# Optimization experiments

Hardware: AMD Instinct MI355X
Metric: run time of the kernel (lower is better)

Reference implementation:

```python
import jax, jax.numpy as jnp
import numpy as np

N, D, H, DZ, R, K, M = 50000, 256, 4, 64, 4, 32, 2
NE, NT = 1600000, 100000
LAM2, LAM3, LAMM = 1.0, 0.5, 1.0
BETA2, BETA3, BETAM = 1.0, 1.0, 1.0
GCLIP, SCLIP, DAMP, EPS = 1.0, 10.0, 0.9999, 1e-5


def _ln(x, gamma, bias):
    mu = x.mean(-1, keepdims=True)
    v = ((x - mu) ** 2).mean(-1, keepdims=True)
    return gamma * (x - mu) / jnp.sqrt(v + EPS) + bias


def _seg_lse(s, idx, n):
    # segment logsumexp over rows of s [E,H] grouped by idx -> [n,H]; 0 for empty segments
    m = jnp.full((n,) + s.shape[1:], -jnp.inf, s.dtype).at[idx].max(s)
    ms = jnp.where(jnp.isfinite(m), m, 0.0)
    z = jnp.zeros((n,) + s.shape[1:], s.dtype).at[idx].add(jnp.exp(s - ms[idx]))
    return jnp.where(z > 0, ms + jnp.log(jnp.maximum(z, 1e-30)), 0.0)


def _energy(X, gamma, bias, W_Q2, W_K2, W_Q3, W_K3, T_tau, W_Qm, W_Km, B_mem,
            c2, u2, c3, u3, v3, tt):
    G = _ln(X, gamma, bias)
    # pairwise (2nd order) attention energy over edges
    Q2 = jnp.einsum('nd,hzd->nhz', G, W_Q2)
    K2 = jnp.einsum('nd,hzd->nhz', G, W_K2)
    s2 = BETA2 * jnp.einsum('ehz,ehz->eh', Q2[c2], K2[u2])
    e = -(LAM2 / BETA2) * _seg_lse(s2, c2, N).sum()
    # motif (3rd order) energy over triples with learned motif tensor T_tau
    Q3 = jnp.einsum('nd,hzd->nhz', G, W_Q3).reshape(N, H, R, DZ)
    K3 = jnp.einsum('nd,hzd->nhz', G, W_K3).reshape(N, H, R, DZ)
    s3 = BETA3 * jnp.einsum('thrz,thrz,thrz,thrz->th', Q3[c3], K3[u3], K3[v3], T_tau[tt])
    e += -(LAM3 / BETA3) * _seg_lse(s3, c3, N).sum()
    # Hopfield-style memory retrieval energy
    Qm = jnp.einsum('nd,hzd->nhz', G, W_Qm)
    Km = jnp.einsum('kd,hzd->hkz', B_mem, W_Km)
    sm = BETAM * jnp.einsum('nhz,hkz->nhk', Qm, Km)
    e += -(LAMM / BETAM) * jax.nn.logsumexp(sm, axis=-1).sum()
    return e


def setup_inputs():
    key = jax.random.key(0)
    ks = jax.random.split(key, 16)
    xav2 = (2.0 / (DZ + D)) ** 0.5
    xav3 = 0.5 * (2.0 / (R * DZ + D)) ** 0.5
    return {
        'X': jax.random.normal(ks[0], (N, D), jnp.float32),
        'c2': jax.random.randint(ks[1], (NE,), 0, N),
        'u2': jax.random.randint(ks[2], (NE,), 0, N),
        'c3': jax.random.randint(ks[3], (NT,), 0, N),
        'u3': jax.random.randint(ks[4], (NT,), 0, N),
        'v3': jax.random.randint(ks[5], (NT,), 0, N),
        't_tau': jax.random.randint(ks[6], (NT,), 0, M),
        'batch': jnp.zeros((N,), jnp.int64) if jax.config.jax_enable_x64 else jnp.zeros((N,), jnp.int32),
        'step_size': jnp.ones((), jnp.float32),
        'gamma': jnp.ones((D,), jnp.float32),
        'bias': jnp.zeros((D,), jnp.float32),
        'W_Q2': jax.random.normal(ks[7], (H, DZ, D), jnp.float32) * xav2,
        'W_K2': jax.random.normal(ks[8], (H, DZ, D), jnp.float32) * xav2,
        'W_Q3': jax.random.normal(ks[9], (H, R * DZ, D), jnp.float32) * xav3,
        'W_K3': jax.random.normal(ks[10], (H, R * DZ, D), jnp.float32) * xav3,
        'T_tau': jax.random.normal(ks[11], (M, H, R, DZ), jnp.float32) * 0.02,
        'W_Qm': jax.random.normal(ks[12], (H, DZ, D), jnp.float32) * 0.5 * xav2,
        'W_Km': jax.random.normal(ks[13], (H, DZ, D), jnp.float32) * 0.5 * xav2,
        'B_mem': jax.random.normal(ks[14], (K, D), jnp.float32) / (D ** 0.5),
    }


def reference(X, c2, u2, c3, u3, v3, t_tau, batch, step_size, gamma, bias,
              W_Q2, W_K2, W_Q3, W_K3, T_tau, W_Qm, W_Km, B_mem):
    E, gX = jax.value_and_grad(_energy)(
        X, gamma, bias, W_Q2, W_K2, W_Q3, W_K3, T_tau, W_Qm, W_Km, B_mem,
        c2, u2, c3, u3, v3, t_tau)
    gn = jnp.linalg.norm(gX, axis=-1, keepdims=True)
    gX = gX * (GCLIP / jnp.maximum(gn, GCLIP))
    Xn = X - step_size * DAMP * gX
    sn = jnp.linalg.norm(Xn, axis=-1, keepdims=True)
    Xn = Xn * (SCLIP / jnp.maximum(sn, SCLIP))
    return Xn, E
```

## Files before the change

### kernel.cpp

```cpp
#include <hip/hip_runtime.h>
#include <math.h>

#define N_NODES 50000
#define D_DIM   256
#define H_HEADS 4
#define NE_EDGES 1600000
#define NT_TRIS  100000

#define LAM2  1.0f
#define LAM3  0.5f
#define LAMM  1.0f
#define GCLIP 1.0f
#define SCLIP 10.0f
#define DAMP  0.9999f
#define EPSLN 1e-5f

typedef short bf16x8 __attribute__((ext_vector_type(8)));
typedef float f32x4  __attribute__((ext_vector_type(4)));

__device__ __forceinline__ float b2f(unsigned short u) {
  return __uint_as_float(((unsigned)u) << 16);
}
__device__ __forceinline__ unsigned short f2b(float f) {
  unsigned u = __float_as_uint(f);
  return (unsigned short)((u + 0x7fffu + ((u >> 16) & 1u)) >> 16);
}
__device__ __forceinline__ bf16x8 ld8(const unsigned short* p) {
  union { uint4 u; bf16x8 v; } t;
  t.u = *(const uint4*)p;
  return t.v;
}
__device__ __forceinline__ void ld4f(const unsigned short* p, float* o) {
  uint2 t = *(const uint2*)p;
  o[0] = __uint_as_float((t.x & 0xffffu) << 16);
  o[1] = __uint_as_float((t.x >> 16) << 16);
  o[2] = __uint_as_float((t.y & 0xffffu) << 16);
  o[3] = __uint_as_float((t.y >> 16) << 16);
}

__device__ __forceinline__ float bsum256(float v, volatile float* red) {
  #pragma unroll
  for (int o = 32; o; o >>= 1) v += __shfl_xor(v, o);
  __syncthreads();
  if ((threadIdx.x & 63) == 0) red[threadIdx.x >> 6] = v;
  __syncthreads();
  return red[0] + red[1] + red[2] + red[3];
}

__global__ void zero_buf(float* __restrict__ p, long n) {
  long i = ((long)blockIdx.x * blockDim.x + threadIdx.x) * 4;
  if (i + 3 < n) *(float4*)(p + i) = make_float4(0.f, 0.f, 0.f, 0.f);
  else for (long j = i; j < n; j++) p[j] = 0.f;
}

__global__ __launch_bounds__(256) void ln_fwd(const float* __restrict__ X,
    float* __restrict__ mu_out, float* __restrict__ rstd_out) {
  __shared__ float red[4];
  int n = blockIdx.x, t = threadIdx.x;
  float x = X[(size_t)n * D_DIM + t];
  float mu = bsum256(x, red) * (1.0f / D_DIM);
  float d = x - mu;
  float var = bsum256(d * d, red) * (1.0f / D_DIM);
  if (t == 0) { mu_out[n] = mu; rstd_out[n] = rsqrtf(var + EPSLN); }
}

__global__ void km_build(const float* __restrict__ Bmem, const float* __restrict__ WKm,
                         float* __restrict__ Km) {
  int idx = blockIdx.x * blockDim.x + threadIdx.x;
  if (idx >= 4 * 32 * 64) return;
  int h = idx >> 11, k = (idx >> 6) & 31, z = idx & 63;
  const float* b = Bmem + (size_t)k * D_DIM;
  const float* w = WKm + ((size_t)h * 64 + z) * D_DIM;
  float s = 0.f;
  for (int d = 0; d < D_DIM; d++) s += b[d] * w[d];
  Km[idx] = s;
}

__global__ void conv_all(const float* __restrict__ WQ2, const float* __restrict__ WK2,
                         const float* __restrict__ WQ3, const float* __restrict__ WK3,
                         const float* __restrict__ WQm,
                         unsigned short* __restrict__ wb, unsigned short* __restrict__ wbt) {
  int i = blockIdx.x * 256 + threadIdx.x;
  int r = i >> 8, d = i & 255;
  const float* src; int lr;
  if (r < 256)       { src = WQ2; lr = r; }
  else if (r < 512)  { src = WK2; lr = r - 256; }
  else if (r < 1536) { src = WQ3; lr = r - 512; }
  else if (r < 2560) { src = WK3; lr = r - 1536; }
  else               { src = WQm; lr = r - 2560; }
  unsigned short v = f2b(src[(size_t)lr * 256 + d]);
  wb[i] = v;
  wbt[(((size_t)(r >> 6) * 256 + d) << 6) + (r & 63)] = v;
}

__global__ void hist5(const int* __restrict__ c2, const int* __restrict__ u2,
                      const int* __restrict__ c3, const int* __restrict__ u3,
                      const int* __restrict__ v3, int* __restrict__ cnt) {
  long i = (long)blockIdx.x * blockDim.x + threadIdx.x;
  if (i < NE_EDGES) {
    atomicAdd(&cnt[c2[i]], 1);
    atomicAdd(&cnt[N_NODES + u2[i]], 1);
  }
  if (i < NT_TRIS) {
    atomicAdd(&cnt[2 * N_NODES + c3[i]], 1);
    atomicAdd(&cnt[3 * N_NODES + u3[i]], 1);
    atomicAdd(&cnt[4 * N_NODES + v3[i]], 1);
  }
}

__global__ __launch_bounds__(256) void scan_blk5(const int* __restrict__ cnt,
    int* __restrict__ offs, int* __restrict__ bsum) {
  __shared__ int ws[4];
  int a = blockIdx.y;
  int i = blockIdx.x * 256 + threadIdx.x;
  int lane = threadIdx.x & 63, w = threadIdx.x >> 6;
  int v = (i < N_NODES) ? cnt[a * N_NODES + i] : 0;
  int inc = v;
  #pragma unroll
  for (int o = 1; o < 64; o <<= 1) { int t = __shfl_up(inc, o); if (lane >= o) inc += t; }
  if (lane == 63) ws[w] = inc;
  __syncthreads();
  int wpre = 0;
  for (int k = 0; k < w; k++) wpre += ws[k];
  if (i < N_NODES) offs[(size_t)a * (N_NODES + 1) + i] = wpre + inc - v;
  if (threadIdx.x == 255) bsum[a * 256 + blockIdx.x] = wpre + inc;
}

__global__ __launch_bounds__(256) void scan_top5(int* __restrict__ bsum, int nb,
                                                 int* __restrict__ offs) {
  __shared__ int ws[4];
  int a = blockIdx.x;
  int lane = threadIdx.x & 63, w = threadIdx.x >> 6;
  int v = (threadIdx.x < nb) ? bsum[a * 256 + threadIdx.x] : 0;
  int inc = v;
  #pragma unroll
  for (int o = 1; o < 64; o <<= 1) { int t = __shfl_up(inc, o); if (lane >= o) inc += t; }
  if (lane == 63) ws[w] = inc;
  __syncthreads();
  int wpre = 0;
  for (int k = 0; k < w; k++) wpre += ws[k];
  if (threadIdx.x < nb) bsum[a * 256 + threadIdx.x] = wpre + inc - v;
  if (threadIdx.x == 255) offs[(size_t)a * (N_NODES + 1) + N_NODES] = wpre + inc;
}

__global__ void scan_add5(int* __restrict__ offs, const int* __restrict__ bsum) {
  int a = blockIdx.y;
  int i = blockIdx.x * 256 + threadIdx.x;
  if (i < N_NODES) offs[(size_t)a * (N_NODES + 1) + i] += bsum[a * 256 + blockIdx.x];
}

__global__ void scatter_e2(const int* __restrict__ c2, const int* __restrict__ u2,
                           const int* __restrict__ offs, int* __restrict__ cur,
                           int* __restrict__ adjA, int* __restrict__ adjB) {
  long i = (long)blockIdx.x * blockDim.x + threadIdx.x;
  if (i >= NE_EDGES) return;
  int a = blockIdx.y;
  const int* idx = a ? u2 : c2;
  const int* cmp = a ? c2 : u2;
  int* out = a ? adjB : adjA;
  int c = idx[i];
  int p = atomicAdd(&cur[a * N_NODES + c], 1);
  out[offs[(size_t)a * (N_NODES + 1) + c] + p] = cmp[i];
}

__global__ void scatter_t3(const int* __restrict__ c3, const int* __restrict__ u3,
                           const int* __restrict__ v3, const int* __restrict__ tt,
                           const int* __restrict__ offs, int* __restrict__ cur,
                           int4* __restrict__ oC, int4* __restrict__ oU, int4* __restrict__ oV) {
  long i = (long)blockIdx.x * blockDim.x + threadIdx.x;
  if (i >= NT_TRIS) return;
  int a = blockIdx.y;
  const int* idx = (a == 0) ? c3 : (a == 1) ? u3 : v3;
  const int* fa  = (a == 0) ? u3 : c3;
  const int* fb  = (a == 2) ? u3 : v3;
  int4* out = (a == 0) ? oC : (a == 1) ? oU : oV;
  int c = idx[i];
  int p = atomicAdd(&cur[(2 + a) * N_NODES + c], 1);
  out[offs[(size_t)(2 + a) * (N_NODES + 1) + c] + p] = make_int4((int)i, fa[i], fb[i], tt[i]);
}

__global__ __launch_bounds__(256) void proj_mfma(
    const float* __restrict__ X, const float* __restrict__ mu, const float* __restrict__ rstd,
    const float* __restrict__ gamma, const float* __restrict__ bias,
    const unsigned short* __restrict__ Wb, int wrow0a, int wrow0b,
    unsigned short* dstA, unsigned short* dstB, int ldc) {
  int wrow0 = blockIdx.z ? wrow0b : wrow0a;
  unsigned short* C = blockIdx.z ? dstB : dstA;
  int wid = threadIdx.x >> 6, lane = threadIdx.x & 63;
  int m0 = blockIdx.x * 64 + wid * 16;
  int rl = lane & 15, kg = lane >> 4;
  int arow = min(m0 + rl, N_NODES - 1);
  float am = mu[arow], ars = rstd[arow];
  const float* xp = X + (size_t)arow * 256 + kg * 8;
  const float* gp = gamma + kg * 8;
  const float* bp = bias + kg * 8;
  f32x4 acc[4][4];
  #pragma unroll
  for (int jt = 0; jt < 4; jt++)
    #pragma unroll
    for (int q = 0; q < 4; q++) acc[jt][q] = (f32x4){0, 0, 0, 0};
  for (int k0 = 0; k0 < 256; k0 += 32) {
    float4 xa = *(const float4*)(xp + k0);
    float4 xb = *(const float4*)(xp + k0 + 4);
    float4 ga = *(const float4*)(gp + k0);
    float4 gb = *(const float4*)(gp + k0 + 4);
    float4 ba = *(const float4*)(bp + k0);
    float4 bb = *(const float4*)(bp + k0 + 4);
    bf16x8 af;
    af[0] = (short)f2b(ga.x * (xa.x - am) * ars + ba.x);
    af[1] = (short)f2b(ga.y * (xa.y - am) * ars + ba.y);
    af[2] = (short)f2b(ga.z * (xa.z - am) * ars + ba.z);
    af[3] = (short)f2b(ga.w * (xa.w - am) * ars + ba.w);
    af[4] = (short)f2b(gb.x * (xb.x - am) * ars + bb.x);
    af[5] = (short)f2b(gb.y * (xb.y - am) * ars + bb.y);
    af[6] = (short)f2b(gb.z * (xb.z - am) * ars + bb.z);
    af[7] = (short)f2b(gb.w * (xb.w - am) * ars + bb.w);
    const unsigned short* wbase = Wb + (size_t)(wrow0 + rl) * 256 + k0 + kg * 8;
    #pragma unroll
    for (int jt = 0; jt < 4; jt++) {
      const unsigned short* wp = wbase + (size_t)jt * 64 * 256;
      acc[jt][0] = __builtin_amdgcn_mfma_f32_16x16x32_bf16(af, ld8(wp),            acc[jt][0], 0, 0, 0);
      acc[jt][1] = __builtin_amdgcn_mfma_f32_16x16x32_bf16(af, ld8(wp + 16 * 256), acc[jt][1], 0, 0, 0);
      acc[jt][2] = __builtin_amdgcn_mfma_f32_16x16x32_bf16(af, ld8(wp + 32 * 256), acc[jt][2], 0, 0, 0);
      acc[jt][3] = __builtin_amdgcn_mfma_f32_16x16x32_bf16(af, ld8(wp + 48 * 256), acc[jt][3], 0, 0, 0);
    }
  }
  int cb = kg * 4;
  #pragma unroll
  for (int jt = 0; jt < 4; jt++) {
    #pragma unroll
    for (int r = 0; r < 4; r++) {
      int row = m0 + cb + r;
      if (row < N_NODES) {
        unsigned short* cp = C + (size_t)row * ldc + jt * 64 + rl;
        cp[0]  = f2b(acc[jt][0][r]);
        cp[16] = f2b(acc[jt][1][r]);
        cp[32] = f2b(acc[jt][2][r]);
        cp[48] = f2b(acc[jt][3][r]);
      }
    }
  }
}

__global__ __launch_bounds__(256) void dg_mfma(
    const unsigned short* __restrict__ A, int lda, int kw,
    int s0, int s1, int s2, int s3,
    const unsigned short* __restrict__ WbT, float* __restrict__ out, int accum) {
  __shared__ unsigned short sA[16 * 1032];
  int tid = threadIdx.x;
  int wid = tid >> 6, lane = tid & 63;
  int m0 = blockIdx.x * 16;
  int KWP = kw + 8;
  for (int e = tid * 8; e < 16 * kw; e += 2048) {
    int row = e / kw, col = e - row * kw;
    *(uint4*)&sA[row * KWP + col] = *(const uint4*)&A[(size_t)(m0 + row) * lda + col];
  }
  __syncthreads();
  int rl = lane & 15, kg = lane >> 4;
  int jb = wid * 64;
  f32x4 acc[4];
  #pragma unroll
  for (int dt = 0; dt < 4; dt++) acc[dt] = (f32x4){0, 0, 0, 0};
  const unsigned short* ap = &sA[rl * KWP + kg * 8];
  #pragma unroll 2
  for (int k0 = 0; k0 < kw; k0 += 32) {
    bf16x8 af;
    { union { uint4 u; bf16x8 v; } t; t.u = *(const uint4*)(ap + k0); af = t.v; }
    int k = k0 + kg * 8;
    int sb = (k < 256) ? s0 : (k < 512) ? s1 : (k < 768) ? s2 : s3;
    int sl = sb + ((k & 255) >> 6);
    const unsigned short* wp = WbT + (((size_t)sl * 256 + jb + rl) << 6) + (k & 63);
    #pragma unroll
    for (int dt = 0; dt < 4; dt++)
      acc[dt] = __builtin_amdgcn_mfma_f32_16x16x32_bf16(af, ld8(wp + dt * 16 * 64), acc[dt], 0, 0, 0);
  }
  int cb = kg * 4;
  #pragma unroll
  for (int r = 0; r < 4; r++) {
    int row = m0 + cb + r;
    float* op = out + (size_t)row * 256 + jb + rl;
    #pragma unroll
    for (int dt = 0; dt < 4; dt++) {
      float v = acc[dt][r];
      op[dt * 16] = accum ? op[dt * 16] + v : v;
    }
  }
}

__global__ __launch_bounds__(256) void mem_term_all(const unsigned short* __restrict__ Q,
    const float* __restrict__ Km, unsigned short* __restrict__ dQ, int ldd,
    float* __restrict__ lsem) {
  __shared__ float kmL[4 * 32 * 65 + 1];
  __shared__ float qs[4][260];
  __shared__ float pb[4][33];
  int tid = threadIdx.x;
  int w = tid >> 6, lane = tid & 63;
  for (int i = tid * 4; i < 8192; i += 1024) {
    float4 v = *(const float4*)(Km + i);
    int h = i >> 11, k = (i >> 6) & 31, z = i & 63;
    float* dp = &kmL[(h * 32 + k) * 65 + z];
    dp[0] = v.x; dp[1] = v.y; dp[2] = v.z; dp[3] = v.w;
  }
  int n = blockIdx.x * 4 + w;
  {
    float o4[4];
    ld4f(&Q[(size_t)n * 256 + lane * 4], o4);
    float* qp = &qs[w][lane * 4];
    qp[0] = o4[0]; qp[1] = o4[1]; qp[2] = o4[2]; qp[3] = o4[3];
  }
  __syncthreads();
  int k = lane & 31, half = lane >> 5;
  #pragma unroll
  for (int h = 0; h < 4; h++) {
    const float* kp = &kmL[(h * 32 + k) * 65 + half * 32];
    const float* qp = &qs[w][h * 64 + half * 32];
    float s = 0.f;
    #pragma unroll
    for (int i = 0; i < 32; i++) s += qp[i] * kp[i];
    s += __shfl_xor(s, 32);
    float m = s;
    #pragma unroll
    for (int o = 16; o; o >>= 1) m = fmaxf(m, __shfl_xor(m, o));
    float e = expf(s - m);
    float zs = e;
    #pragma unroll
    for (int o = 16; o; o >>= 1) zs += __shfl_xor(zs, o);
    if (lane < 32) pb[w][k] = e / zs;
    if (lane == 0) lsem[(size_t)n * 4 + h] = m + logf(zs);
    __syncthreads();
    const float* kz = &kmL[h * 32 * 65 + lane];
    float a = 0.f;
    #pragma unroll
    for (int kk = 0; kk < 32; kk++) a += pb[w][kk] * kz[kk * 65];
    dQ[(size_t)n * ldd + h * 64 + lane] = f2b(-LAMM * a);
    __syncthreads();
  }
}

__global__ __launch_bounds__(256) void reduce_add(const float* __restrict__ v, int n,
                                                  float coef, float* __restrict__ Eacc) {
  __shared__ float red[4];
  int i = blockIdx.x * 256 + threadIdx.x;
  float x = (i < n) ? v[i] : 0.f;
  float tot = bsum256(x, red);
  if (threadIdx.x == 0) atomicAdd(Eacc, coef * tot);
}

__global__ __launch_bounds__(256) void edge_fwd_all(const unsigned short* __restrict__ Q,
    const unsigned short* __restrict__ K,
    const int* __restrict__ off, const int* __restrict__ adj,
    float* __restrict__ lse2, unsigned short* __restrict__ dst, int ldd, int coloff) {
  int wid = threadIdx.x >> 6, lane = threadIdx.x & 63;
  int n = blockIdx.x * 4 + wid;
  int beg = off[n], end = off[n + 1];
  int d0 = lane * 4;
  float q[4];
  ld4f(&Q[(size_t)n * 256 + d0], q);
  float m = -1e30f, z = 0.f;
  float a0 = 0.f, a1 = 0.f, a2 = 0.f, a3 = 0.f;
  int e = beg;
  for (; e + 3 < end; e += 4) {
    float kk[4][4], s[4];
    #pragma unroll
    for (int j = 0; j < 4; j++) ld4f(&K[(size_t)adj[e + j] * 256 + d0], kk[j]);
    #pragma unroll
    for (int j = 0; j < 4; j++)
      s[j] = q[0] * kk[j][0] + q[1] * kk[j][1] + q[2] * kk[j][2] + q[3] * kk[j][3];
    #pragma unroll
    for (int o = 1; o <= 8; o <<= 1)
      #pragma unroll
      for (int j = 0; j < 4; j++) s[j] += __shfl_xor(s[j], o);
    float nm = fmaxf(fmaxf(m, fmaxf(s[0], s[1])), fmaxf(s[2], s[3]));
    float sc = expf(m - nm);
    float e0 = expf(s[0] - nm), e1 = expf(s[1] - nm);
    float e2 = expf(s[2] - nm), e3 = expf(s[3] - nm);
    z = z * sc + e0 + e1 + e2 + e3;
    a0 = a0 * sc + e0 * kk[0][0] + e1 * kk[1][0] + e2 * kk[2][0] + e3 * kk[3][0];
    a1 = a1 * sc + e0 * kk[0][1] + e1 * kk[1][1] + e2 * kk[2][1] + e3 * kk[3][1];
    a2 = a2 * sc + e0 * kk[0][2] + e1 * kk[1][2] + e2 * kk[2][2] + e3 * kk[3][2];
    a3 = a3 * sc + e0 * kk[0][3] + e1 * kk[1][3] + e2 * kk[2][3] + e3 * kk[3][3];
    m = nm;
  }
  for (; e < end; e++) {
    int u = adj[e];
    float k[4];
    ld4f(&K[(size_t)u * 256 + d0], k);
    float s = q[0] * k[0] + q[1] * k[1] + q[2] * k[2] + q[3] * k[3];
    s += __shfl_xor(s, 1); s += __shfl_xor(s, 2);
    s += __shfl_xor(s, 4); s += __shfl_xor(s, 8);
    float nm = fmaxf(m, s);
    float sc = expf(m - nm), es = expf(s - nm);
    z = z * sc + es;
    a0 = a0 * sc + es * k[0];
    a1 = a1 * sc + es * k[1];
    a2 = a2 * sc + es * k[2];
    a3 = a3 * sc + es * k[3];
    m = nm;
  }
  float lse = 0.f, inv = 0.f;
  if (end > beg) { lse = m + logf(z); inv = 1.f / z; }
  if ((lane & 15) == 0) lse2[(size_t)n * 4 + (lane >> 4)] = lse;
  ushort4 o;
  o.x = f2b(-LAM2 * a0 * inv);
  o.y = f2b(-LAM2 * a1 * inv);
  o.z = f2b(-LAM2 * a2 * inv);
  o.w = f2b(-LAM2 * a3 * inv);
  *(ushort4*)&dst[(size_t)n * ldd + coloff + d0] = o;
}

__global__ __launch_bounds__(256) void edge_dk_all(const unsigned short* __restrict__ Q,
    const unsigned short* __restrict__ K, const float* __restrict__ lse2,
    const int* __restrict__ off, const int* __restrict__ adj,
    unsigned short* __restrict__ dst, int ldd, int coloff) {
  int wid = threadIdx.x >> 6, lane = threadIdx.x & 63;
  int n = blockIdx.x * 4 + wid;
  int beg = off[n], end = off[n + 1];
  int h = lane >> 4, d0 = lane * 4;
  float k[4];
  ld4f(&K[(size_t)n * 256 + d0], k);
  float a0 = 0.f, a1 = 0.f, a2 = 0.f, a3 = 0.f;
  int e = beg;
  for (; e + 3 < end; e += 4) {
    float qq[4][4], s[4], l[4];
    int cc[4];
    #pragma unroll
    for (int j = 0; j < 4; j++) cc[j] = adj[e + j];
    #pragma unroll
    for (int j = 0; j < 4; j++) ld4f(&Q[(size_t)cc[j] * 256 + d0], qq[j]);
    #pragma unroll
    for (int j = 0; j < 4; j++) l[j] = lse2[(size_t)cc[j] * 4 + h];
    #pragma unroll
    for (int j = 0; j < 4; j++)
      s[j] = qq[j][0] * k[0] + qq[j][1] * k[1] + qq[j][2] * k[2] + qq[j][3] * k[3];
    #pragma unroll
    for (int o = 1; o <= 8; o <<= 1)
      #pragma unroll
      for (int j = 0; j < 4; j++) s[j] += __shfl_xor(s[j], o);
    #pragma unroll
    for (int j = 0; j < 4; j++) {
      float p = expf(s[j] - l[j]);
      a0 += p * qq[j][0]; a1 += p * qq[j][1];
      a2 += p * qq[j][2]; a3 += p * qq[j][3];
    }
  }
  for (; e < end; e++) {
    int c = adj[e];
    float q[4];
    ld4f(&Q[(size_t)c * 256 + d0], q);
    float s = q[0] * k[0] + q[1] * k[1] + q[2] * k[2] + q[3] * k[3];
    s += __shfl_xor(s, 1); s += __shfl_xor(s, 2);
    s += __shfl_xor(s, 4); s += __shfl_xor(s, 8);
    float p = expf(s - lse2[(size_t)c * 4 + h]);
    a0 += p * q[0]; a1 += p * q[1]; a2 += p * q[2]; a3 += p * q[3];
  }
  ushort4 o;
  o.x = f2b(-LAM2 * a0);
  o.y = f2b(-LAM2 * a1);
  o.z = f2b(-LAM2 * a2);
  o.w = f2b(-LAM2 * a3);
  *(ushort4*)&dst[(size_t)n * ldd + coloff + d0] = o;
}

__global__ __launch_bounds__(256) void tri_score(const unsigned short* __restrict__ Q,
    const unsigned short* __restrict__ K, const float* __restrict__ Tt,
    const int* __restrict__ c3, const int* __restrict__ u3, const int* __restrict__ v3,
    const int* __restrict__ tt, int h, float* __restrict__ s3) {
  int t = blockIdx.x * 16 + (threadIdx.x >> 4);
  int g = threadIdx.x & 15;
  int c = c3[t], u = u3[t], v = v3[t], mt = tt[t];
  float s = 0.f;
  #pragma unroll
  for (int i = 0; i < 4; i++) {
    float qv[4], av[4], bv[4];
    ld4f(&Q[(size_t)c * 256 + i * 64 + g * 4], qv);
    ld4f(&K[(size_t)u * 256 + i * 64 + g * 4], av);
    ld4f(&K[(size_t)v * 256 + i * 64 + g * 4], bv);
    float4 w = *(const float4*)&Tt[(((size_t)mt * 4 + h) * 4 + i) * 64 + g * 4];
    s += qv[0] * av[0] * bv[0] * w.x + qv[1] * av[1] * bv[1] * w.y
       + qv[2] * av[2] * bv[2] * w.z + qv[3] * av[3] * bv[3] * w.w;
  }
  #pragma unroll
  for (int o = 8; o; o >>= 1) s += __shfl_xor(s, o);
  if (g == 0) s3[t] = s;
}

__global__ __launch_bounds__(256) void tri_lse(const float* __restrict__ s3,
    const int* __restrict__ off, const int4* __restrict__ ids4,
    float* __restrict__ lse3, float* __restrict__ Eacc) {
  __shared__ float red[4];
  int n = blockIdx.x * 256 + threadIdx.x;
  float l = 0.f;
  if (n < N_NODES) {
    int beg = off[n], end = off[n + 1];
    if (end > beg) {
      float m = -1e30f;
      for (int e = beg; e < end; e++) m = fmaxf(m, s3[ids4[e].x]);
      float z = 0.f;
      for (int e = beg; e < end; e++) z += expf(s3[ids4[e].x] - m);
      l = m + logf(z);
    }
    lse3[n] = l;
  }
  float tot = bsum256(l, red);
  if (threadIdx.x == 0) atomicAdd(Eacc, -LAM3 * tot);
}

__global__ __launch_bounds__(256) void tri_grad(const unsigned short* __restrict__ Q,
    const unsigned short* __restrict__ K, const float* __restrict__ Tt, int h,
    const float* __restrict__ s3, const float* __restrict__ lse,
    const int* __restrict__ offc, const int4* __restrict__ idsC,
    const int* __restrict__ offu, const int4* __restrict__ idsU,
    const int* __restrict__ offv, const int4* __restrict__ idsV,
    unsigned short* __restrict__ dst, int ldd, int colbase, int dkoff, int mode) {
  int wid = threadIdx.x >> 6, lane = threadIdx.x & 63;
  int n = blockIdx.x * 4 + wid;
  int d0 = lane * 4;
  if (mode & 1) {
    float a0 = 0.f, a1 = 0.f, a2 = 0.f, a3 = 0.f;
    float lsen = lse[n];
    for (int e = offc[n]; e < offc[n + 1]; e++) {
      int4 pk = idsC[e];
      float p = expf(s3[pk.x] - lsen);
      float av[4], bv[4];
      ld4f(&K[(size_t)pk.y * 256 + d0], av);
      ld4f(&K[(size_t)pk.z * 256 + d0], bv);
      float4 w = *(const float4*)&Tt[((size_t)pk.w * 4 + h) * 256 + d0];
      a0 += p * av[0] * bv[0] * w.x;
      a1 += p * av[1] * bv[1] * w.y;
      a2 += p * av[2] * bv[2] * w.z;
      a3 += p * av[3] * bv[3] * w.w;
    }
    ushort4 o;
    o.x = f2b(-LAM3 * a0); o.y = f2b(-LAM3 * a1);
    o.z = f2b(-LAM3 * a2); o.w = f2b(-LAM3 * a3);
    *(ushort4*)&dst[(size_t)n * ldd + colbase + d0] = o;
  }
  if (mode & 2) {
    float a0 = 0.f, a1 = 0.f, a2 = 0.f, a3 = 0.f;
    for (int e = offu[n]; e < offu[n + 1]; e++) {
      int4 pk = idsU[e];
      float p = expf(s3[pk.x] - lse[pk.y]);
      float qv[4], bv[4];
      ld4f(&Q[(size_t)pk.y * 256 + d0], qv);
      ld4f(&K[(size_t)pk.z * 256 + d0], bv);
      float4 w = *(const float4*)&Tt[((size_t)pk.w * 4 + h) * 256 + d0];
      a0 += p * qv[0] * bv[0] * w.x;
      a1 += p * qv[1] * bv[1] * w.y;
      a2 += p * qv[2] * bv[2] * w.z;
      a3 += p * qv[3] * bv[3] * w.w;
    }
    for (int e = offv[n]; e < offv[n + 1]; e++) {
      int4 pk = idsV[e];
      float p = expf(s3[pk.x] - lse[pk.y]);
      float qv[4], av[4];
      ld4f(&Q[(size_t)pk.y * 256 + d0], qv);
      ld4f(&K[(size_t)pk.z * 256 + d0], av);
      float4 w = *(const float4*)&Tt[((size_t)pk.w * 4 + h) * 256 + d0];
      a0 += p * qv[0] * av[0] * w.x;
      a1 += p * qv[1] * av[1] * w.y;
      a2 += p * qv[2] * av[2] * w.z;
      a3 += p * qv[3] * av[3] * w.w;
    }
    ushort4 o;
    o.x = f2b(-LAM3 * a0); o.y = f2b(-LAM3 * a1);
    o.z = f2b(-LAM3 * a2); o.w = f2b(-LAM3 * a3);
    *(ushort4*)&dst[(size_t)n * ldd + colbase + dkoff + d0] = o;
  }
}

__global__ __launch_bounds__(256) void final_update(const float* __restrict__ X,
    const float* dG, const float* __restrict__ gamma,
    const float* __restrict__ mu, const float* __restrict__ rstd,
    const float* __restrict__ step_size, float* out) {
  __shared__ float red[4];
  int n = blockIdx.x, t = threadIdx.x;
  float x = X[(size_t)n * D_DIM + t];
  float mun = mu[n], rs = rstd[n];
  float xhat = (x - mun) * rs;
  float a = dG[(size_t)n * D_DIM + t] * gamma[t];
  float h1 = bsum256(a, red) * (1.0f / D_DIM);
  float h2 = bsum256(a * xhat, red) * (1.0f / D_DIM);
  float dx = rs * (a - h1 - xhat * h2);
  float gn2 = bsum256(dx * dx, red);
  float gsc = GCLIP / fmaxf(sqrtf(gn2), GCLIP);
  float xn = x - step_size[0] * DAMP * dx * gsc;
  float sn2 = bsum256(xn * xn, red);
  float ssc = SCLIP / fmaxf(sqrtf(sn2), SCLIP);
  out[(size_t)n * D_DIM + t] = xn * ssc;
}

__global__ void write_E(const float* __restrict__ Eacc, float* __restrict__ out) {
  if (threadIdx.x == 0) out[(size_t)N_NODES * D_DIM] = Eacc[0];
}


extern "C" void kernel_launch(void* const* d_in, const int* in_sizes, int n_in,
                              void* d_out, int out_size, void* d_ws, size_t ws_size,
                              hipStream_t stream) {
  const float* X     = (const float*)d_in[0];
  const int*   c2    = (const int*)d_in[1];
  const int*   u2    = (const int*)d_in[2];
  const int*   c3    = (const int*)d_in[3];
  const int*   u3    = (const int*)d_in[4];
  const int*   v3    = (const int*)d_in[5];
  const int*   tt    = (const int*)d_in[6];
  const float* step  = (const float*)d_in[8];
  const float* gamma = (const float*)d_in[9];
  const float* bias  = (const float*)d_in[10];
  const float* WQ2   = (const float*)d_in[11];
  const float* WK2   = (const float*)d_in[12];
  const float* WQ3   = (const float*)d_in[13];
  const float* WK3   = (const float*)d_in[14];
  const float* Ttau  = (const float*)d_in[15];
  const float* WQm   = (const float*)d_in[16];
  const float* WKm   = (const float*)d_in[17];
  const float* Bmem  = (const float*)d_in[18];
  float* out = (float*)d_out;

  size_t off = 0;
  auto allocB = [&](size_t bytes) {
    void* p = (char*)d_ws + off;
    off += (bytes + 1023) & ~(size_t)1023;
    return p;
  };
  auto Z = [&](void* p, long cnt4) {
    zero_buf<<<(int)((cnt4 / 4 + 255) / 256), 256, 0, stream>>>((float*)p, cnt4);
  };

  bool quad = ws_size >= (size_t)175 * 1024 * 1024;
  bool dual = !quad && ws_size >= (size_t)128 * 1024 * 1024;
  int  DW   = quad ? 1024 : (dual ? 512 : 256);

  unsigned short* Qb  = (unsigned short*)allocB((size_t)N_NODES * 256 * 2);
  unsigned short* Kb  = (unsigned short*)allocB((size_t)N_NODES * 256 * 2);
  unsigned short* Db  = (unsigned short*)allocB((size_t)N_NODES * DW * 2);
  float* s3   = (float*)allocB((size_t)NT_TRIS * 4);
  float* lse  = (float*)allocB((size_t)N_NODES * 4);
  float* lse2 = (float*)allocB((size_t)N_NODES * 4 * 4);
  float* mu   = (float*)allocB((size_t)N_NODES * 4);
  float* rstd = (float*)allocB((size_t)N_NODES * 4);
  float* Km   = (float*)allocB(4 * 32 * 64 * 4);
  float* Eacc = (float*)allocB(1024);
  unsigned short* Wb  = (unsigned short*)allocB((size_t)2816 * 256 * 2);
  unsigned short* WbT = (unsigned short*)allocB((size_t)2816 * 256 * 2);
  int*  cnt   = (int*)allocB((size_t)5 * N_NODES * 4);
  int*  bsum  = (int*)allocB(5 * 256 * 4);
  int*  offs  = (int*)allocB((size_t)5 * (N_NODES + 1) * 4);
  int*  adjc2 = (int*)allocB((size_t)NE_EDGES * 4);
  int*  adju2 = (int*)allocB((size_t)NE_EDGES * 4);
  int4* ids4c3 = (int4*)allocB((size_t)NT_TRIS * 16);
  int4* ids4u3 = (int4*)allocB((size_t)NT_TRIS * 16);
  int4* ids4v3 = (int4*)allocB((size_t)NT_TRIS * 16);

  const int NB  = (N_NODES + 255) / 256;
  const int NB4 = (N_NODES * 4 + 255) / 256;
  const int GN  = (N_NODES + 63) / 64;
  const int GND = N_NODES / 16;
  const int GW  = N_NODES / 4;
  const int gbE = (NE_EDGES + 255) / 256;
  const int gbT = (NT_TRIS + 255) / 256;

  int* offc2 = offs;
  int* offu2 = offs + (N_NODES + 1);
  int* offc3 = offs + 2 * (N_NODES + 1);
  int* offu3 = offs + 3 * (N_NODES + 1);
  int* offv3 = offs + 4 * (N_NODES + 1);

  Z(cnt, (long)5 * N_NODES);
  hist5<<<gbE, 256, 0, stream>>>(c2, u2, c3, u3, v3, cnt);
  scan_blk5<<<dim3(NB, 5), 256, 0, stream>>>(cnt, offs, bsum);
  scan_top5<<<5, 256, 0, stream>>>(bsum, NB, offs);
  scan_add5<<<dim3(NB, 5), 256, 0, stream>>>(offs, bsum);
  Z(cnt, (long)5 * N_NODES);
  scatter_e2<<<dim3(gbE, 2), 256, 0, stream>>>(c2, u2, offs, cnt, adjc2, adju2);
  scatter_t3<<<dim3(gbT, 3), 256, 0, stream>>>(c3, u3, v3, tt, offs, cnt, ids4c3, ids4u3, ids4v3);

  ln_fwd<<<N_NODES, 256, 0, stream>>>(X, mu, rstd);
  km_build<<<32, 256, 0, stream>>>(Bmem, WKm, Km);
  conv_all<<<2816, 256, 0, stream>>>(WQ2, WK2, WQ3, WK3, WQm, Wb, WbT);
  Z(Eacc, 256);

  if (quad) {
    proj_mfma<<<dim3(GN, 1, 1), 256, 0, stream>>>(X, mu, rstd, gamma, bias, Wb, 2560, 0, Qb, Qb, 256);
    mem_term_all<<<GW, 256, 0, stream>>>(Qb, Km, Db, DW, lse2);
    reduce_add<<<NB4, 256, 0, stream>>>(lse2, N_NODES * 4, -LAMM, Eacc);
    proj_mfma<<<dim3(GN, 1, 2), 256, 0, stream>>>(X, mu, rstd, gamma, bias, Wb, 0, 256, Qb, Kb, 256);
    edge_fwd_all<<<GW, 256, 0, stream>>>(Qb, Kb, offc2, adjc2, lse2, Db, DW, 256);
    reduce_add<<<NB4, 256, 0, stream>>>(lse2, N_NODES * 4, -LAM2, Eacc);
    edge_dk_all<<<GW, 256, 0, stream>>>(Qb, Kb, lse2, offu2, adju2, Db, DW, 512);
    dg_mfma<<<GND, 256, 0, stream>>>(Db, DW, 768, 40, 0, 4, 0, WbT, out, 0);

    for (int p = 0; p < 2; p++) {
      for (int hh = 0; hh < 2; hh++) {
        int h = 2 * p + hh;
        proj_mfma<<<dim3(GN, 1, 2), 256, 0, stream>>>(X, mu, rstd, gamma, bias, Wb,
            512 + h * 256, 1536 + h * 256, Qb, Kb, 256);
        tri_score<<<NT_TRIS / 16, 256, 0, stream>>>(Qb, Kb, Ttau, c3, u3, v3, tt, h, s3);
        tri_lse<<<NB, 256, 0, stream>>>(s3, offc3, ids4c3, lse, Eacc);
        tri_grad<<<GW, 256, 0, stream>>>(Qb, Kb, Ttau, h, s3, lse,
            offc3, ids4c3, offu3, ids4u3, offv3, ids4v3, Db, DW, hh * 512, 256, 3);
      }
      dg_mfma<<<GND, 256, 0, stream>>>(Db, DW, 1024,
          8 + 8 * p, 24 + 8 * p, 12 + 8 * p, 28 + 8 * p, WbT, out, 1);
    }
  } else {
    proj_mfma<<<dim3(GN, 1, 1), 256, 0, stream>>>(X, mu, rstd, gamma, bias, Wb, 2560, 0, Qb, Qb, 256);
    mem_term_all<<<GW, 256, 0, stream>>>(Qb, Km, Db, DW, lse2);
    reduce_add<<<NB4, 256, 0, stream>>>(lse2, N_NODES * 4, -LAMM, Eacc);
    dg_mfma<<<GND, 256, 0, stream>>>(Db, DW, 256, 40, 0, 0, 0, WbT, out, 0);

    proj_mfma<<<dim3(GN, 1, 2), 256, 0, stream>>>(X, mu, rstd, gamma, bias, Wb, 0, 256, Qb, Kb, 256);
    edge_fwd_all<<<GW, 256, 0, stream>>>(Qb, Kb, offc2, adjc2, lse2, Db, DW, 0);
    reduce_add<<<NB4, 256, 0, stream>>>(lse2, N_NODES * 4, -LAM2, Eacc);
    if (dual) {
      edge_dk_all<<<GW, 256, 0, stream>>>(Qb, Kb, lse2, offu2, adju2, Db, DW, 256);
      dg_mfma<<<GND, 256, 0, stream>>>(Db, DW, 512, 0, 4, 0, 0, WbT, out, 1);
    } else {
      dg_mfma<<<GND, 256, 0, stream>>>(Db, DW, 256, 0, 0, 0, 0, WbT, out, 1);
      edge_dk_all<<<GW, 256, 0, stream>>>(Qb, Kb, lse2, offu2, adju2, Db, DW, 0);
      dg_mfma<<<GND, 256, 0, stream>>>(Db, DW, 256, 4, 0, 0, 0, WbT, out, 1);
    }

    for (int h = 0; h < H_HEADS; h++) {
      proj_mfma<<<dim3(GN, 1, 2), 256, 0, stream>>>(X, mu, rstd, gamma, bias, Wb,
          512 + h * 256, 1536 + h * 256, Qb, Kb, 256);
      tri_score<<<NT_TRIS / 16, 256, 0, stream>>>(Qb, Kb, Ttau, c3, u3, v3, tt, h, s3);
      tri_lse<<<NB, 256, 0, stream>>>(s3, offc3, ids4c3, lse, Eacc);
      if (dual) {
        tri_grad<<<GW, 256, 0, stream>>>(Qb, Kb, Ttau, h, s3, lse,
            offc3, ids4c3, offu3, ids4u3, offv3, ids4v3, Db, DW, 0, 256, 3);
        dg_mfma<<<GND, 256, 0, stream>>>(Db, DW, 512, 8 + h * 4, 24 + h * 4, 0, 0, WbT, out, 1);
      } else {
        tri_grad<<<GW, 256, 0, stream>>>(Qb, Kb, Ttau, h, s3, lse,
            offc3, ids4c3, offu3, ids4u3, offv3, ids4v3, Db, DW, 0, 0, 1);
        dg_mfma<<<GND, 256, 0, stream>>>(Db, DW, 256, 8 + h * 4, 0, 0, 0, WbT, out, 1);
        tri_grad<<<GW, 256, 0, stream>>>(Qb, Kb, Ttau, h, s3, lse,
            offc3, ids4c3, offu3, ids4u3, offv3, ids4v3, Db, DW, 0, 0, 2);
        dg_mfma<<<GND, 256, 0, stream>>>(Db, DW, 256, 24 + h * 4, 0, 0, 0, WbT, out, 1);
      }
    }
  }

  final_update<<<N_NODES, 256, 0, stream>>>(X, out, gamma, mu, rstd, step, out);
  write_E<<<1, 64, 0, stream>>>(Eacc, out);
}
```

Baseline: 2.460 ms.

## Retile dg_mfma to 64-row blocks with shared-memory weight staging

New measurement: 2.156 ms. 1.14x faster.

```diff
diff --git a/kernel.cpp b/kernel.cpp
--- a/kernel.cpp
+++ b/kernel.cpp
@@ -246,43 +246,74 @@
     const unsigned short* __restrict__ A, int lda, int kw,
     int s0, int s1, int s2, int s3,
     const unsigned short* __restrict__ WbT, float* __restrict__ out, int accum) {
-  __shared__ unsigned short sA[16 * 1032];
+  __shared__ unsigned short sW[256 * 64];
+  __shared__ unsigned short sA[64 * 64];
   int tid = threadIdx.x;
   int wid = tid >> 6, lane = tid & 63;
-  int m0 = blockIdx.x * 16;
-  int KWP = kw + 8;
-  for (int e = tid * 8; e < 16 * kw; e += 2048) {
-    int row = e / kw, col = e - row * kw;
-    *(uint4*)&sA[row * KWP + col] = *(const uint4*)&A[(size_t)(m0 + row) * lda + col];
-  }
-  __syncthreads();
+  int m0 = blockIdx.x * 64;
   int rl = lane & 15, kg = lane >> 4;
   int jb = wid * 64;
-  f32x4 acc[4];
-  #pragma unroll
-  for (int dt = 0; dt < 4; dt++) acc[dt] = (f32x4){0, 0, 0, 0};
-  const unsigned short* ap = &sA[rl * KWP + kg * 8];
-  #pragma unroll 2
-  for (int k0 = 0; k0 < kw; k0 += 32) {
-    bf16x8 af;
-    { union { uint4 u; bf16x8 v; } t; t.u = *(const uint4*)(ap + k0); af = t.v; }
-    int k = k0 + kg * 8;
-    int sb = (k < 256) ? s0 : (k < 512) ? s1 : (k < 768) ? s2 : s3;
-    int sl = sb + ((k & 255) >> 6);
-    const unsigned short* wp = WbT + (((size_t)sl * 256 + jb + rl) << 6) + (k & 63);
-    #pragma unroll
-    for (int dt = 0; dt < 4; dt++)
-      acc[dt] = __builtin_amdgcn_mfma_f32_16x16x32_bf16(af, ld8(wp + dt * 16 * 64), acc[dt], 0, 0, 0);
+  f32x4 acc[4][4];
+  #pragma unroll
+  for (int rg = 0; rg < 4; rg++)
+    #pragma unroll
+    for (int dt = 0; dt < 4; dt++) acc[rg][dt] = (f32x4){0, 0, 0, 0};
+  for (int kt = 0; kt < kw; kt += 64) {
+    int sb = (kt < 256) ? s0 : (kt < 512) ? s1 : (kt < 768) ? s2 : s3;
+    int sl = sb + ((kt & 255) >> 6);
+    const unsigned short* wsrc = WbT + ((size_t)sl << 14);
+    #pragma unroll
+    for (int i = 0; i < 8; i++) {
+      int u = tid + (i << 8);
+      int col = u >> 3, k8 = u & 7;
+      *(uint4*)&sW[(col << 6) + ((k8 ^ (col & 7)) << 3)] = *(const uint4*)(wsrc + (u << 3));
+    }
+    #pragma unroll
+    for (int i = 0; i < 2; i++) {
+      int u = tid + (i << 8);
+      int row = u >> 3, k8 = u & 7;
+      int gr = min(m0 + row, N_NODES - 1);
+      *(uint4*)&sA[(row << 6) + ((k8 ^ (row & 7)) << 3)] =
+          *(const uint4*)&A[(size_t)gr * lda + kt + (k8 << 3)];
+    }
+    __syncthreads();
+    #pragma unroll
+    for (int ks = 0; ks < 2; ks++) {
+      int k8a = (ks << 2) + kg;
+      int swz = (k8a ^ (rl & 7)) << 3;
+      bf16x8 wf[4];
+      #pragma unroll
+      for (int dt = 0; dt < 4; dt++) {
+        int col = jb + dt * 16 + rl;
+        union { uint4 u; bf16x8 v; } t;
+        t.u = *(const uint4*)&sW[(col << 6) + swz];
+        wf[dt] = t.v;
+      }
+      #pragma unroll
+      for (int rg = 0; rg < 4; rg++) {
+        union { uint4 u; bf16x8 v; } t;
+        t.u = *(const uint4*)&sA[((rg * 16 + rl) << 6) + swz];
+        #pragma unroll
+        for (int dt = 0; dt < 4; dt++)
+          acc[rg][dt] = __builtin_amdgcn_mfma_f32_16x16x32_bf16(t.v, wf[dt], acc[rg][dt], 0, 0, 0);
+      }
+    }
+    __syncthreads();
   }
   int cb = kg * 4;
   #pragma unroll
-  for (int r = 0; r < 4; r++) {
-    int row = m0 + cb + r;
-    float* op = out + (size_t)row * 256 + jb + rl;
-    #pragma unroll
-    for (int dt = 0; dt < 4; dt++) {
-      float v = acc[dt][r];
-      op[dt * 16] = accum ? op[dt * 16] + v : v;
+  for (int rg = 0; rg < 4; rg++) {
+    #pragma unroll
+    for (int r = 0; r < 4; r++) {
+      int row = m0 + rg * 16 + cb + r;
+      if (row < N_NODES) {
+        float* op = out + (size_t)row * 256 + jb + rl;
+        #pragma unroll
+        for (int dt = 0; dt < 4; dt++) {
+          float v = acc[rg][dt][r];
+          op[dt * 16] = accum ? op[dt * 16] + v : v;
+        }
+      }
     }
   }
 }
@@ -655,7 +686,7 @@
   const int NB  = (N_NODES + 255) / 256;
   const int NB4 = (N_NODES * 4 + 255) / 256;
   const int GN  = (N_NODES + 63) / 64;
-  const int GND = N_NODES / 16;
+  const int GND = (N_NODES + 63) / 64;
   const int GW  = N_NODES / 4;
   const int gbE = (NE_EDGES + 255) / 256;
   const int gbT = (NT_TRIS + 255) / 256;
```
